# Kernel optimization log

Measured on AMD Instinct MI355X. Metric: run time of the kernel, lower is better.

## Reference

```python
import jax, jax.numpy as jnp
import numpy as np

N = 50000      # node_num
C = 64         # num_classes
G = 3          # number of metapath graphs (len(g))
E = 1200000    # edges per metapath graph
L = 2          # layers (PLPConv propagation steps)
D = 256        # input feature dim (feat_dims[0])
H = 256        # hidden_dim


def setup_inputs() -> dict:
    key = jax.random.key(0)
    ks = jax.random.split(key, 13)
    features0 = jax.random.normal(ks[0], (N, D), jnp.float32)
    labels = jax.random.randint(ks[1], (N,), 0, C)
    labels_one_hot = jax.nn.one_hot(labels, C, dtype=jnp.float32)
    # label_init: soft labels, rows on the simplex
    label_init = jax.nn.softmax(jax.random.normal(ks[2], (N, C), jnp.float32), axis=-1)
    train_mask = (jax.random.uniform(ks[3], (N, 1)) < 0.5).astype(jnp.float32)
    src = jax.random.randint(ks[4], (G, E), 0, N, dtype=jnp.int32)
    dst = jax.random.randint(ks[5], (G, E), 0, N, dtype=jnp.int32)
    # per-layer, per-graph learned edge logits (xavier-ish small init)
    e_edges = 0.1 * jax.random.normal(ks[6], (L, G, E), jnp.float32)
    attention = 0.5 * jax.random.normal(ks[7], (N, G), jnp.float32)
    alpha = 0.5 * jax.random.normal(ks[8], (N, 1), jnp.float32)
    W1 = jax.random.normal(ks[9], (D, H), jnp.float32) / np.sqrt(D)
    b1 = jnp.zeros((H,), jnp.float32)
    W2 = jax.random.normal(ks[10], (H, C), jnp.float32) / np.sqrt(H)
    b2 = jnp.zeros((C,), jnp.float32)
    return {"features0": features0, "label_init": label_init,
            "labels_one_hot": labels_one_hot, "train_mask": train_mask,
            "src": src, "dst": dst, "e_edges": e_edges,
            "attention": attention, "alpha": alpha,
            "W1": W1, "b1": b1, "W2": W2, "b2": b2}


def _edge_softmax(e, dst, n):
    # softmax of per-edge scalar over incoming edges of each dst node
    m = jax.ops.segment_max(e, dst, num_segments=n)
    a = jnp.exp(e - m[dst])
    s = jax.ops.segment_sum(a, dst, num_segments=n)
    return a / s[dst]


def reference(features0, label_init, labels_one_hot, train_mask,
              src, dst, e_edges, attention, alpha, W1, b1, W2, b2):
    n = label_init.shape[0]
    masked_label = 1.0 - train_mask            # (~masked).float(), [N,1]
    masked_oh = labels_one_hot * train_mask    # labels_one_hot * masked, [N,C]

    # Label propagation over each metapath graph (PLPConv stack, activation=None)
    h_prime = []
    for i in range(G):
        h = label_init
        for l in range(L):
            a = _edge_softmax(e_edges[l, i], dst[i], n)         # [E]
            msg = h[src[i]] * a[:, None]                        # gather-mul [E,C]
            h = jax.ops.segment_sum(msg, dst[i], num_segments=n)  # scatter-sum [N,C]
            h = h * masked_label + masked_oh                    # clamp train labels
        h_prime.append(h)
    x = jnp.stack(h_prime, axis=-1)                             # [N,C,G]

    att_mp = jax.nn.softmax(attention, axis=1)                  # [N,G]
    logits_lp = jnp.einsum('ncg,ng->nc', x, att_mp)             # [N,C]

    # MLP2 (2 layers, dropout=0): relu(x W1 + b1) W2 + b2
    hm = jax.nn.relu(features0 @ W1 + b1)
    logits_ns = hm @ W2 + b2                                    # [N,C]

    logits = jax.nn.sigmoid(alpha) * logits_lp + jax.nn.sigmoid(-alpha) * logits_ns
    return (logits, logits_lp, logits_ns)
```

## Files before the change

kernel.cpp:

```cpp
#include <hip/hip_runtime.h>
#include <hip/hip_bf16.h>

#define NN 50000
#define CC 64
#define GG 3
#define EE 1200000
#define LL 2
#define DD 256
#define HH 256
#define NB 196
#define NBLK 293
#define NBK (GG * NB)
#define BKCAP 8192
#define CH 16384
#define CBLK 74


__device__ __forceinline__ ushort f2bf(float f) {
    unsigned b = __float_as_uint(f);
    return (ushort)((b + 0x7fffu + ((b >> 16) & 1u)) >> 16);
}
__device__ __forceinline__ float bf2f(unsigned u) {
    return __uint_as_float(u << 16);
}

typedef __attribute__((ext_vector_type(8))) short s8v;
typedef __attribute__((ext_vector_type(4))) float f4v;

template<int NWM, int NWN, bool A_FP32, bool OUT_RELU_BF16>
__global__ __launch_bounds__(256) void mfma_gemm_kernel(
    const void* __restrict__ Av, const ushort* __restrict__ Bt,
    const float* __restrict__ bias, void* __restrict__ Cv, int M, int Nc)
{
    static_assert(NWM * NWN == 4, "4 waves per block");
    const int tid = threadIdx.x;
    const int w = tid >> 6;
    const int l = tid & 63;
    const int wm = w / NWN;
    const int wn = w % NWN;
    const int r0 = blockIdx.x * (NWM * 64) + wm * 64;
    const int c0 = blockIdx.y * (NWN * 64) + wn * 64;
    const int lrow = l & 15;
    const int lk = (l >> 4) << 3;

    f4v acc[4][4] = {};

    for (int k0 = 0; k0 < 256; k0 += 32) {
        s8v a[4], b[4];
        #pragma unroll
        for (int i = 0; i < 4; i++) {
            int row = r0 + lrow + 16 * i;
            row = (row < M) ? row : (M - 1);
            if constexpr (A_FP32) {
                const float* Af = (const float*)Av;
                const float4* p = (const float4*)(Af + (size_t)row * 256 + k0 + lk);
                float4 f0 = p[0], f1 = p[1];
                union { ushort u[8]; s8v v; } t;
                t.u[0] = f2bf(f0.x); t.u[1] = f2bf(f0.y);
                t.u[2] = f2bf(f0.z); t.u[3] = f2bf(f0.w);
                t.u[4] = f2bf(f1.x); t.u[5] = f2bf(f1.y);
                t.u[6] = f2bf(f1.z); t.u[7] = f2bf(f1.w);
                a[i] = t.v;
            } else {
                const ushort* Ab = (const ushort*)Av;
                a[i] = *(const s8v*)(Ab + (size_t)row * 256 + k0 + lk);
            }
        }
        #pragma unroll
        for (int j = 0; j < 4; j++) {
            int col = c0 + lrow + 16 * j;
            b[j] = *(const s8v*)(Bt + (size_t)col * 256 + k0 + lk);
        }
        #pragma unroll
        for (int i = 0; i < 4; i++)
            #pragma unroll
            for (int j = 0; j < 4; j++)
                acc[i][j] = __builtin_amdgcn_mfma_f32_16x16x32_bf16(
                    a[i], b[j], acc[i][j], 0, 0, 0);
    }

    #pragma unroll
    for (int i = 0; i < 4; i++) {
        #pragma unroll
        for (int r = 0; r < 4; r++) {
            int row = r0 + 16 * i + (l >> 4) * 4 + r;
            if (row >= M) continue;
            #pragma unroll
            for (int j = 0; j < 4; j++) {
                int col = c0 + 16 * j + lrow;
                float v = acc[i][j][r] + bias[col];
                if constexpr (OUT_RELU_BF16) {
                    v = fmaxf(v, 0.f);
                    ((ushort*)Cv)[(size_t)row * Nc + col] = f2bf(v);
                } else {
                    ((float*)Cv)[(size_t)row * Nc + col] = v;
                }
            }
        }
    }
}

__global__ void wcvt_kernel(const float* __restrict__ W1,
                            const float* __restrict__ W2,
                            ushort* __restrict__ Wt1, ushort* __restrict__ Wt2)
{
    int idx = blockIdx.x * 256 + threadIdx.x;
    if (idx < 256 * 256) {
        int n = idx >> 8, k = idx & 255;
        Wt1[idx] = f2bf(W1[k * 256 + n]);
    } else {
        int i = idx - 256 * 256;
        if (i < 64 * 256) {
            int n = i >> 8, k = i & 255;
            Wt2[i] = f2bf(W2[k * 64 + n]);
        }
    }
}

__global__ __launch_bounds__(256) void prep_kernel(
    const float* __restrict__ label_init, const float* __restrict__ labels_oh,
    const float* __restrict__ train_mask, ushort* __restrict__ lab_bf,
    short* __restrict__ mid)
{
    int b = blockIdx.x;
    if (b < 3125) {
        int i = b * 256 + threadIdx.x;
        int v = i >> 4;
        int c4 = (i & 15) * 4;
        float4 f = ((const float4*)label_init)[i];
        ushort4 u;
        u.x = f2bf(f.x); u.y = f2bf(f.y); u.z = f2bf(f.z); u.w = f2bf(f.w);
        int pl = c4 >> 5;
        *(ushort4*)(lab_bf + (size_t)pl * NN * 32 + (size_t)v * 32 + (c4 & 31)) = u;
    } else {
        int t = threadIdx.x;
        int v = (b - 3125) * 16 + (t >> 4);
        int sl = t & 15;
        if (v < NN) {
            float4 f = ((const float4*)(labels_oh + (size_t)v * 64))[sl];
            float p = (float)(sl * 4);
            float s = f.x * p + f.y * (p + 1.f) + f.z * (p + 2.f) + f.w * (p + 3.f);
            s += __shfl_xor(s, 1); s += __shfl_xor(s, 2);
            s += __shfl_xor(s, 4); s += __shfl_xor(s, 8);
            if (sl == 0) {
                float tm = train_mask[v];
                mid[v] = (tm > 0.5f) ? (short)(s + 0.5f) : (short)-1;
            }
        }
    }
}

__global__ __launch_bounds__(256) void bhist_kernel(
    const int* __restrict__ dst, int* __restrict__ bcnt)
{
    int blk = blockIdx.x;
    int g = blk / NBLK;
    int bi = blk - g * NBLK;
    int base = bi * 4096;
    __shared__ int cnt[NB];
    int t = threadIdx.x;
    if (t < NB) cnt[t] = 0;
    __syncthreads();
    #pragma unroll
    for (int k = 0; k < 16; k++) {
        int e = base + k * 256 + t;
        if (e < EE) atomicAdd(&cnt[dst[g * EE + e] >> 8], 1);
    }
    __syncthreads();
    if (t < NB && cnt[t] > 0) atomicAdd(&bcnt[g * NB + t], cnt[t]);
}

__global__ void scan_bucket(const int* __restrict__ bcnt, int* __restrict__ bs)
{
    __shared__ int sd[256];
    __shared__ int s_run;
    int t = threadIdx.x;
    if (t == 0) s_run = 0;
    __syncthreads();
    for (int base = 0; base < NBK; base += 256) {
        int i = base + t;
        int v = (i < NBK) ? bcnt[i] : 0;
        sd[t] = v;
        __syncthreads();
        for (int o = 1; o < 256; o <<= 1) {
            int x = (t >= o) ? sd[t - o] : 0;
            __syncthreads();
            sd[t] += x;
            __syncthreads();
        }
        int run = s_run;
        __syncthreads();
        if (i < NBK) bs[i] = run + sd[t] - v;
        if (t == 255) s_run = run + sd[255];
        __syncthreads();
    }
    if (t == 0) bs[NBK] = GG * EE;
}

__global__ __launch_bounds__(1024) void binA_kernel(
    const int* __restrict__ dst, const int* __restrict__ src,
    const float* __restrict__ e_edges, const int* __restrict__ bucket_start,
    int* __restrict__ fill, uint2* __restrict__ staging)
{
    int blk = blockIdx.x;
    int g = blk / CBLK;
    int bi = blk - g * CBLK;
    int base = bi * CH;
    __shared__ uint2 rec[CH];
    __shared__ int cnt[NB];
    __shared__ int lstart[NB];
    __shared__ int cur[NB];
    __shared__ int gbase[NB];
    __shared__ int sd[256];
    int t = threadIdx.x;
    if (t < NB) cnt[t] = 0;
    __syncthreads();

    int myd[16];
    #pragma unroll
    for (int k = 0; k < 16; k++) {
        int e = base + k * 1024 + t;
        int d = (e < EE) ? dst[g * EE + e] : -1;
        myd[k] = d;
        if (d >= 0) atomicAdd(&cnt[d >> 8], 1);
    }
    __syncthreads();

    if (t < 256) sd[t] = (t < NB) ? cnt[t] : 0;
    __syncthreads();
    for (int o = 1; o < 256; o <<= 1) {
        int x = (t < 256 && t >= o) ? sd[t - o] : 0;
        __syncthreads();
        if (t < 256) sd[t] += x;
        __syncthreads();
    }
    if (t < NB) {
        int c = cnt[t];
        int ls = sd[t] - c;
        lstart[t] = ls;
        cur[t] = ls;
        int fo = (c > 0) ? atomicAdd(&fill[g * NB + t], c) : 0;
        gbase[t] = bucket_start[g * NB + t] + fo;
    }
    __syncthreads();

    #pragma unroll
    for (int k = 0; k < 16; k++) {
        int d = myd[k];
        if (d >= 0) {
            int e = base + k * 1024 + t;
            int pos = atomicAdd(&cur[d >> 8], 1);
            int idxg = g * EE + e;
            uint2 r;
            r.x = ((unsigned)f2bf(e_edges[idxg]) << 16) |
                  (unsigned)f2bf(e_edges[(size_t)(GG + g) * EE + e]);
            r.y = ((unsigned)src[idxg] << 16) | (unsigned)(d & 255);
            rec[pos] = r;
        }
    }
    __syncthreads();

    int w = t >> 6, lane = t & 63;
    for (int b = w; b < NB; b += 16) {
        int c = cnt[b];
        int ls = lstart[b];
        uint2* dp = staging + gbase[b];
        for (int i = lane; i < c; i += 64) dp[i] = rec[ls + i];
    }
}

__global__ __launch_bounds__(1024) void bucket_kernel(
    const uint2* __restrict__ staging, const int* __restrict__ bucket_start,
    int* __restrict__ row_start, unsigned* __restrict__ packed0,
    unsigned* __restrict__ packed1)
{
    int blk = blockIdx.x;
    int g = blk / NB;
    int bucket = blk - g * NB;
    int bn = bucket << 8;
    int bnodes = min(256, NN - bn);
    int sbase = bucket_start[blk];
    int n = bucket_start[blk + 1] - sbase;
    int segStart = sbase - g * EE;
    const uint2* st = staging + sbase;

    __shared__ int hist[256];
    __shared__ int sd[256];
    __shared__ int cur[256];
    __shared__ float sm[512];
    __shared__ ushort ab0[BKCAP];
    __shared__ ushort ab1[BKCAP];
    __shared__ ushort sb[BKCAP];
    int t = threadIdx.x;
    if (t < 256) hist[t] = 0;
    if (t < 512) sm[t] = 0.f;
    __syncthreads();

    for (int i = t; i < n; i += 1024) {
        uint2 r = st[i];
        int dl = r.y & 0xff;
        atomicAdd(&hist[dl], 1);
        atomicAdd(&sm[dl], __expf(bf2f(r.x >> 16)));
        atomicAdd(&sm[256 + dl], __expf(bf2f(r.x & 0xffffu)));
    }
    __syncthreads();

    if (t < 256) sd[t] = hist[t];
    __syncthreads();
    for (int o = 1; o < 256; o <<= 1) {
        int x = (t < 256 && t >= o) ? sd[t - o] : 0;
        __syncthreads();
        if (t < 256) sd[t] += x;
        __syncthreads();
    }
    if (t < 256) {
        cur[t] = sd[t] - hist[t];
        if (t < bnodes)
            row_start[(size_t)g * (NN + 1) + bn + t] = segStart + sd[t] - hist[t];
        if (hist[t] > 0) {
            sm[t] = 1.f / sm[t];
            sm[256 + t] = 1.f / sm[256 + t];
        }
    }
    if (bucket == NB - 1 && t == 0) row_start[(size_t)g * (NN + 1) + NN] = EE;
    __syncthreads();

    for (int i = t; i < n; i += 1024) {
        uint2 r = st[i];
        int dl = r.y & 0xff;
        int pos = atomicAdd(&cur[dl], 1);
        ab0[pos] = f2bf(__expf(bf2f(r.x >> 16)) * sm[dl]);
        ab1[pos] = f2bf(__expf(bf2f(r.x & 0xffffu)) * sm[256 + dl]);
        sb[pos] = (ushort)(r.y >> 16);
    }
    __syncthreads();

    for (int i = t; i < n; i += 1024) {
        unsigned s = sb[i];
        packed0[(size_t)sbase + i] = ((unsigned)ab0[i] << 16) | s;
        packed1[(size_t)sbase + i] = ((unsigned)ab1[i] << 16) | s;
    }
}

__device__ __forceinline__ void tile_pass(unsigned packed, int cnt,
        const ushort* __restrict__ plane, unsigned loff, int sub, float acc[4])
{
    for (int q0 = 0; q0 < cnt; q0 += 32) {
        uint2 gv[4]; float w[4];
        #pragma unroll
        for (int u = 0; u < 4; u++) {
            unsigned pkq = __shfl(packed, q0 + 8 * u + sub);
            w[u] = __uint_as_float(pkq & 0xffff0000u);
            gv[u] = *(const uint2*)((const char*)plane +
                                    (((pkq & 0xffffu) << 6) | loff));
        }
        #pragma unroll
        for (int u = 0; u < 4; u++) {
            acc[0] = fmaf(__uint_as_float(gv[u].x << 16),          w[u], acc[0]);
            acc[1] = fmaf(__uint_as_float(gv[u].x & 0xffff0000u),  w[u], acc[1]);
            acc[2] = fmaf(__uint_as_float(gv[u].y << 16),          w[u], acc[2]);
            acc[3] = fmaf(__uint_as_float(gv[u].y & 0xffff0000u),  w[u], acc[3]);
        }
    }
}

__global__ __launch_bounds__(256) void prop0_kernel(
    const ushort* __restrict__ lab_bf, const short* __restrict__ mid,
    const int* __restrict__ row_start, const unsigned* __restrict__ packed0,
    ushort* __restrict__ h_buf)
{
    int wid = (blockIdx.x * blockDim.x + threadIdx.x) >> 6;
    int lane = threadIdx.x & 63;
    if (wid >= GG * NN) return;
    int g = wid / NN;
    int v = wid - g * NN;
    const int* rs = row_start + (size_t)g * (NN + 1);
    int s = rs[v], tE = rs[v + 1];
    const unsigned* pk = packed0 + (size_t)g * EE;
    const ushort* pl0 = lab_bf;
    const ushort* pl1 = lab_bf + (size_t)NN * 32;

    unsigned loff = (lane & 7) << 3;
    int sub = lane >> 3;
    float a0[4] = {}, a1[4] = {};
    for (int base = s; base < tE; base += 64) {
        int j = base + lane;
        unsigned packed = (j < tE) ? pk[j] : 0u;
        int cnt = min(64, tE - base);
        tile_pass(packed, cnt, pl0, loff, sub, a0);
        tile_pass(packed, cnt, pl1, loff, sub, a1);
    }
    #pragma unroll
    for (int c = 0; c < 4; c++) {
        a0[c] += __shfl_xor(a0[c], 8);
        a0[c] += __shfl_xor(a0[c], 16);
        a0[c] += __shfl_xor(a0[c], 32);
        a1[c] += __shfl_xor(a1[c], 8);
        a1[c] += __shfl_xor(a1[c], 16);
        a1[c] += __shfl_xor(a1[c], 32);
    }
    int m = mid[v];
    float ml = (m < 0) ? 1.f : 0.f;
    ushort* hg = h_buf + (size_t)g * NN * 64;
    int cb = (lane & 7) * 4;
    if (lane < 8) {
        ushort4 o;
        o.x = f2bf(a0[0] * ml + ((cb + 0 == m) ? 1.f : 0.f));
        o.y = f2bf(a0[1] * ml + ((cb + 1 == m) ? 1.f : 0.f));
        o.z = f2bf(a0[2] * ml + ((cb + 2 == m) ? 1.f : 0.f));
        o.w = f2bf(a0[3] * ml + ((cb + 3 == m) ? 1.f : 0.f));
        *(ushort4*)(hg + (size_t)v * 32 + cb) = o;
    } else if (lane < 16) {
        int cc = cb + 32;
        ushort4 o;
        o.x = f2bf(a1[0] * ml + ((cc + 0 == m) ? 1.f : 0.f));
        o.y = f2bf(a1[1] * ml + ((cc + 1 == m) ? 1.f : 0.f));
        o.z = f2bf(a1[2] * ml + ((cc + 2 == m) ? 1.f : 0.f));
        o.w = f2bf(a1[3] * ml + ((cc + 3 == m) ? 1.f : 0.f));
        *(ushort4*)(hg + (size_t)NN * 32 + (size_t)v * 32 + cb) = o;
    }
}

__global__ __launch_bounds__(256) void final_kernel(
    const ushort* __restrict__ h_buf, const short* __restrict__ mid,
    const float* __restrict__ attention, const float* __restrict__ alpha,
    const int* __restrict__ row_start, const unsigned* __restrict__ packed1,
    const float* __restrict__ out_ns, float* __restrict__ out_logits,
    float* __restrict__ out_lp)
{
    int wid = (blockIdx.x * blockDim.x + threadIdx.x) >> 6;
    int lane = threadIdx.x & 63;
    if (wid >= NN) return;
    int v = wid;
    float t0 = attention[v * 3], t1 = attention[v * 3 + 1], t2 = attention[v * 3 + 2];
    float mxa = fmaxf(t0, fmaxf(t1, t2));
    float e0 = __expf(t0 - mxa), e1 = __expf(t1 - mxa), e2 = __expf(t2 - mxa);
    float ainv = 1.f / (e0 + e1 + e2);
    float attw[3] = {e0 * ainv, e1 * ainv, e2 * ainv};

    unsigned loff = (lane & 7) << 3;
    int sub = lane >> 3;
    float w0[4] = {}, w1[4] = {};
    #pragma unroll
    for (int g = 0; g < GG; g++) {
        const int* rs = row_start + (size_t)g * (NN + 1);
        int s = rs[v], tE = rs[v + 1];
        const unsigned* pk = packed1 + (size_t)g * EE;
        const ushort* hp0 = h_buf + (size_t)g * NN * 64;
        const ushort* hp1 = hp0 + (size_t)NN * 32;
        float b0[4] = {}, b1[4] = {};
        for (int base = s; base < tE; base += 64) {
            int j = base + lane;
            unsigned packed = (j < tE) ? pk[j] : 0u;
            int cnt = min(64, tE - base);
            tile_pass(packed, cnt, hp0, loff, sub, b0);
            tile_pass(packed, cnt, hp1, loff, sub, b1);
        }
        float aw = attw[g];
        #pragma unroll
        for (int c = 0; c < 4; c++) {
            w0[c] = fmaf(aw, b0[c], w0[c]);
            w1[c] = fmaf(aw, b1[c], w1[c]);
        }
    }
    #pragma unroll
    for (int c = 0; c < 4; c++) {
        w0[c] += __shfl_xor(w0[c], 8);
        w0[c] += __shfl_xor(w0[c], 16);
        w0[c] += __shfl_xor(w0[c], 32);
        w1[c] += __shfl_xor(w1[c], 8);
        w1[c] += __shfl_xor(w1[c], 16);
        w1[c] += __shfl_xor(w1[c], 32);
    }
    int m = mid[v];
    float ml = (m < 0) ? 1.f : 0.f;
    if (lane < 16) {
        int pl = lane >> 3;
        int cb = (lane & 7) * 4 + pl * 32;
        float4 lpv;
        if (pl == 0) {
            lpv.x = w0[0] * ml + ((cb + 0 == m) ? 1.f : 0.f);
            lpv.y = w0[1] * ml + ((cb + 1 == m) ? 1.f : 0.f);
            lpv.z = w0[2] * ml + ((cb + 2 == m) ? 1.f : 0.f);
            lpv.w = w0[3] * ml + ((cb + 3 == m) ? 1.f : 0.f);
        } else {
            lpv.x = w1[0] * ml + ((cb + 0 == m) ? 1.f : 0.f);
            lpv.y = w1[1] * ml + ((cb + 1 == m) ? 1.f : 0.f);
            lpv.z = w1[2] * ml + ((cb + 2 == m) ? 1.f : 0.f);
            lpv.w = w1[3] * ml + ((cb + 3 == m) ? 1.f : 0.f);
        }
        size_t o = (size_t)v * 64 + cb;
        *(float4*)(out_lp + o) = lpv;
        float al = alpha[v];
        float sg = 1.f / (1.f + __expf(-al));
        float4 ns = *(const float4*)(out_ns + o);
        float4 lg;
        lg.x = sg * lpv.x + (1.f - sg) * ns.x;
        lg.y = sg * lpv.y + (1.f - sg) * ns.y;
        lg.z = sg * lpv.z + (1.f - sg) * ns.z;
        lg.w = sg * lpv.w + (1.f - sg) * ns.w;
        *(float4*)(out_logits + o) = lg;
    }
}

extern "C" void kernel_launch(void* const* d_in, const int* in_sizes, int n_in,
                              void* d_out, int out_size, void* d_ws, size_t ws_size,
                              hipStream_t stream)
{
    const float* features0  = (const float*)d_in[0];
    const float* label_init = (const float*)d_in[1];
    const float* labels_oh  = (const float*)d_in[2];
    const float* train_mask = (const float*)d_in[3];
    const int*   src        = (const int*)d_in[4];
    const int*   dst        = (const int*)d_in[5];
    const float* e_edges    = (const float*)d_in[6];
    const float* attention  = (const float*)d_in[7];
    const float* alpha      = (const float*)d_in[8];
    const float* W1         = (const float*)d_in[9];
    const float* b1         = (const float*)d_in[10];
    const float* W2         = (const float*)d_in[11];
    const float* b2         = (const float*)d_in[12];

    float* out        = (float*)d_out;
    float* out_logits = out;
    float* out_lp     = out + (size_t)NN * CC;
    float* out_ns     = out + 2 * (size_t)NN * CC;

    char* base = (char*)d_ws;
    size_t off = 0;
    auto alloc = [&](size_t bytes) -> void* {
        void* p = base + off;
        off = (off + bytes + 255) & ~(size_t)255;
        return p;
    };
    int*      bcnt         = (int*)alloc((size_t)NBK * sizeof(int));
    int*      fill         = (int*)alloc((size_t)NBK * sizeof(int));
    size_t    zero_bytes   = off;
    int*      bucket_start = (int*)alloc((size_t)(NBK + 1) * sizeof(int));
    int*      row_start    = (int*)alloc((size_t)GG * (NN + 1) * sizeof(int));
    uint2*    staging      = (uint2*)alloc((size_t)GG * EE * sizeof(uint2));
    unsigned* packed0      = (unsigned*)alloc((size_t)GG * EE * sizeof(unsigned));
    unsigned* packed1      = (unsigned*)alloc((size_t)GG * EE * sizeof(unsigned));
    ushort*   h_buf        = (ushort*)alloc((size_t)GG * NN * CC * sizeof(ushort));
    ushort*   lab_bf       = (ushort*)alloc((size_t)NN * CC * sizeof(ushort));
    short*    mid          = (short*)alloc((size_t)NN * sizeof(short));

    ushort* Wt1   = (ushort*)packed0;
    ushort* Wt2   = Wt1 + 256 * 256;
    ushort* hm_bf = (ushort*)staging;

    wcvt_kernel<<<(256 * 256 + 64 * 256) / 256, 256, 0, stream>>>(W1, W2, Wt1, Wt2);
    mfma_gemm_kernel<2, 2, true, true><<<dim3((NN + 127) / 128, 2), 256, 0, stream>>>(
        features0, Wt1, b1, hm_bf, NN, HH);
    mfma_gemm_kernel<4, 1, false, false><<<dim3((NN + 255) / 256, 1), 256, 0, stream>>>(
        hm_bf, Wt2, b2, out_ns, NN, CC);

    prep_kernel<<<6250, 256, 0, stream>>>(label_init, labels_oh, train_mask,
                                          lab_bf, mid);

    hipMemsetAsync(bcnt, 0, zero_bytes, stream);
    bhist_kernel<<<GG * NBLK, 256, 0, stream>>>(dst, bcnt);
    scan_bucket<<<1, 256, 0, stream>>>(bcnt, bucket_start);
    binA_kernel<<<GG * CBLK, 1024, 0, stream>>>(
        dst, src, e_edges, bucket_start, fill, staging);
    bucket_kernel<<<GG * NB, 1024, 0, stream>>>(
        staging, bucket_start, row_start, packed0, packed1);

    prop0_kernel<<<((size_t)GG * NN * 64 + 255) / 256, 256, 0, stream>>>(
        lab_bf, mid, row_start, packed0, h_buf);

    final_kernel<<<((size_t)NN * 64 + 255) / 256, 256, 0, stream>>>(
        h_buf, mid, attention, alpha, row_start, packed1,
        out_ns, out_logits, out_lp);
}
```

Measured before the change: 512.3 us.

## Drop histogram pass with fixed-capacity buckets; split propagation per graph and half-plane

Removes the separate dst-histogram kernel. Edges are binned into fixed-capacity staging slots per bucket (BKCAP), and the prefix scan runs after binning on the fill counts. The propagation kernels now assign one wave per (graph, node, 32-channel half-plane), with block indices interleaved so both halves of a node run close together. The final kernel writes per-graph attention-weighted partials that a new combine kernel sums. This trades an extra pass over the edges and a single serial gather loop for more parallel work, more launches, and an extra round-trip of partial results through memory. It also relies on no bucket exceeding BKCAP edges, which the random inputs make likely.

```diff
diff --git a/kernel.cpp b/kernel.cpp
--- a/kernel.cpp
+++ b/kernel.cpp
@@ -9,7 +9,6 @@
 #define DD 256
 #define HH 256
 #define NB 196
-#define NBLK 293
 #define NBK (GG * NB)
 #define BKCAP 8192
 #define CH 16384
@@ -150,27 +149,7 @@
     }
 }
 
-__global__ __launch_bounds__(256) void bhist_kernel(
-    const int* __restrict__ dst, int* __restrict__ bcnt)
-{
-    int blk = blockIdx.x;
-    int g = blk / NBLK;
-    int bi = blk - g * NBLK;
-    int base = bi * 4096;
-    __shared__ int cnt[NB];
-    int t = threadIdx.x;
-    if (t < NB) cnt[t] = 0;
-    __syncthreads();
-    #pragma unroll
-    for (int k = 0; k < 16; k++) {
-        int e = base + k * 256 + t;
-        if (e < EE) atomicAdd(&cnt[dst[g * EE + e] >> 8], 1);
-    }
-    __syncthreads();
-    if (t < NB && cnt[t] > 0) atomicAdd(&bcnt[g * NB + t], cnt[t]);
-}
-
-__global__ void scan_bucket(const int* __restrict__ bcnt, int* __restrict__ bs)
+__global__ void scan_bucket(const int* __restrict__ fill, int* __restrict__ bs)
 {
     __shared__ int sd[256];
     __shared__ int s_run;
@@ -179,7 +158,7 @@
     __syncthreads();
     for (int base = 0; base < NBK; base += 256) {
         int i = base + t;
-        int v = (i < NBK) ? bcnt[i] : 0;
+        int v = (i < NBK) ? fill[i] : 0;
         sd[t] = v;
         __syncthreads();
         for (int o = 1; o < 256; o <<= 1) {
@@ -199,8 +178,8 @@
 
 __global__ __launch_bounds__(1024) void binA_kernel(
     const int* __restrict__ dst, const int* __restrict__ src,
-    const float* __restrict__ e_edges, const int* __restrict__ bucket_start,
-    int* __restrict__ fill, uint2* __restrict__ staging)
+    const float* __restrict__ e_edges, int* __restrict__ fill,
+    uint2* __restrict__ staging)
 {
     int blk = blockIdx.x;
     int g = blk / CBLK;
@@ -240,7 +219,7 @@
         lstart[t] = ls;
         cur[t] = ls;
         int fo = (c > 0) ? atomicAdd(&fill[g * NB + t], c) : 0;
-        gbase[t] = bucket_start[g * NB + t] + fo;
+        gbase[t] = (g * NB + t) * BKCAP + fo;
     }
     __syncthreads();
 
@@ -264,25 +243,25 @@
     for (int b = w; b < NB; b += 16) {
         int c = cnt[b];
         int ls = lstart[b];
-        uint2* dp = staging + gbase[b];
+        uint2* dp = staging + (size_t)gbase[b];
         for (int i = lane; i < c; i += 64) dp[i] = rec[ls + i];
     }
 }
 
 __global__ __launch_bounds__(1024) void bucket_kernel(
-    const uint2* __restrict__ staging, const int* __restrict__ bucket_start,
-    int* __restrict__ row_start, unsigned* __restrict__ packed0,
-    unsigned* __restrict__ packed1)
+    const uint2* __restrict__ staging, const int* __restrict__ fill,
+    const int* __restrict__ out_start, int* __restrict__ row_start,
+    unsigned* __restrict__ packed0, unsigned* __restrict__ packed1)
 {
     int blk = blockIdx.x;
     int g = blk / NB;
     int bucket = blk - g * NB;
     int bn = bucket << 8;
     int bnodes = min(256, NN - bn);
-    int sbase = bucket_start[blk];
-    int n = bucket_start[blk + 1] - sbase;
-    int segStart = sbase - g * EE;
-    const uint2* st = staging + sbase;
+    int n = fill[blk];
+    int obase = out_start[blk];
+    int segStart = obase - g * EE;
+    const uint2* st = staging + (size_t)blk * BKCAP;
 
     __shared__ int hist[256];
     __shared__ int sd[256];
@@ -337,8 +316,8 @@
 
     for (int i = t; i < n; i += 1024) {
         unsigned s = sb[i];
-        packed0[(size_t)sbase + i] = ((unsigned)ab0[i] << 16) | s;
-        packed1[(size_t)sbase + i] = ((unsigned)ab1[i] << 16) | s;
+        packed0[(size_t)obase + i] = ((unsigned)ab0[i] << 16) | s;
+        packed1[(size_t)obase + i] = ((unsigned)ab1[i] << 16) | s;
     }
 }
 
@@ -369,138 +348,130 @@
     const int* __restrict__ row_start, const unsigned* __restrict__ packed0,
     ushort* __restrict__ h_buf)
 {
-    int wid = (blockIdx.x * blockDim.x + threadIdx.x) >> 6;
-    int lane = threadIdx.x & 63;
-    if (wid >= GG * NN) return;
-    int g = wid / NN;
-    int v = wid - g * NN;
+    int blk = blockIdx.x;
+    int x = blk & 7, q = blk >> 3;
+    int pl = x & 1;
+    int bIdx = q * 4 + (x >> 1);
+    int w = threadIdx.x >> 6, lane = threadIdx.x & 63;
+    int gv = bIdx * 4 + w;
+    int g = gv / NN;
+    int v = gv - g * NN;
     const int* rs = row_start + (size_t)g * (NN + 1);
     int s = rs[v], tE = rs[v + 1];
     const unsigned* pk = packed0 + (size_t)g * EE;
-    const ushort* pl0 = lab_bf;
-    const ushort* pl1 = lab_bf + (size_t)NN * 32;
+    const ushort* plane = lab_bf + (size_t)pl * NN * 32;
 
     unsigned loff = (lane & 7) << 3;
     int sub = lane >> 3;
-    float a0[4] = {}, a1[4] = {};
+    float a[4] = {};
     for (int base = s; base < tE; base += 64) {
         int j = base + lane;
-        unsigned packed = (j < tE) ? pk[j] : 0u;
+        unsigned packed = (j < tE) ? __builtin_nontemporal_load(pk + j) : 0u;
         int cnt = min(64, tE - base);
-        tile_pass(packed, cnt, pl0, loff, sub, a0);
-        tile_pass(packed, cnt, pl1, loff, sub, a1);
+        tile_pass(packed, cnt, plane, loff, sub, a);
     }
     #pragma unroll
     for (int c = 0; c < 4; c++) {
-        a0[c] += __shfl_xor(a0[c], 8);
-        a0[c] += __shfl_xor(a0[c], 16);
-        a0[c] += __shfl_xor(a0[c], 32);
-        a1[c] += __shfl_xor(a1[c], 8);
-        a1[c] += __shfl_xor(a1[c], 16);
-        a1[c] += __shfl_xor(a1[c], 32);
+        a[c] += __shfl_xor(a[c], 8);
+        a[c] += __shfl_xor(a[c], 16);
+        a[c] += __shfl_xor(a[c], 32);
     }
     int m = mid[v];
     float ml = (m < 0) ? 1.f : 0.f;
-    ushort* hg = h_buf + (size_t)g * NN * 64;
-    int cb = (lane & 7) * 4;
     if (lane < 8) {
+        int cb = lane * 4;
+        int cg = pl * 32 + cb;
         ushort4 o;
-        o.x = f2bf(a0[0] * ml + ((cb + 0 == m) ? 1.f : 0.f));
-        o.y = f2bf(a0[1] * ml + ((cb + 1 == m) ? 1.f : 0.f));
-        o.z = f2bf(a0[2] * ml + ((cb + 2 == m) ? 1.f : 0.f));
-        o.w = f2bf(a0[3] * ml + ((cb + 3 == m) ? 1.f : 0.f));
-        *(ushort4*)(hg + (size_t)v * 32 + cb) = o;
-    } else if (lane < 16) {
-        int cc = cb + 32;
-        ushort4 o;
-        o.x = f2bf(a1[0] * ml + ((cc + 0 == m) ? 1.f : 0.f));
-        o.y = f2bf(a1[1] * ml + ((cc + 1 == m) ? 1.f : 0.f));
-        o.z = f2bf(a1[2] * ml + ((cc + 2 == m) ? 1.f : 0.f));
-        o.w = f2bf(a1[3] * ml + ((cc + 3 == m) ? 1.f : 0.f));
-        *(ushort4*)(hg + (size_t)NN * 32 + (size_t)v * 32 + cb) = o;
-    }
-}
-
-__global__ __launch_bounds__(256) void final_kernel(
-    const ushort* __restrict__ h_buf, const short* __restrict__ mid,
-    const float* __restrict__ attention, const float* __restrict__ alpha,
+        o.x = f2bf(a[0] * ml + ((cg + 0 == m) ? 1.f : 0.f));
+        o.y = f2bf(a[1] * ml + ((cg + 1 == m) ? 1.f : 0.f));
+        o.z = f2bf(a[2] * ml + ((cg + 2 == m) ? 1.f : 0.f));
+        o.w = f2bf(a[3] * ml + ((cg + 3 == m) ? 1.f : 0.f));
+        *(ushort4*)(h_buf + ((size_t)(g * 2 + pl)) * NN * 32 + (size_t)v * 32 + cb) = o;
+    }
+}
+
+__global__ __launch_bounds__(256) void finalp_kernel(
+    const ushort* __restrict__ h_buf, const float* __restrict__ attention,
     const int* __restrict__ row_start, const unsigned* __restrict__ packed1,
-    const float* __restrict__ out_ns, float* __restrict__ out_logits,
-    float* __restrict__ out_lp)
-{
-    int wid = (blockIdx.x * blockDim.x + threadIdx.x) >> 6;
-    int lane = threadIdx.x & 63;
-    if (wid >= NN) return;
-    int v = wid;
+    float* __restrict__ partial)
+{
+    int blk = blockIdx.x;
+    int x = blk & 7, q = blk >> 3;
+    int combo, vblk;
+    if (x < 2) {
+        if (q >= 6250) return;
+        combo = x; vblk = q;
+    } else if (x < 6) {
+        combo = x; vblk = q;
+    } else {
+        if (q >= 6250) return;
+        combo = x - 6; vblk = 6250 + q;
+    }
+    int g = combo >> 1, pl = combo & 1;
+    int w = threadIdx.x >> 6, lane = threadIdx.x & 63;
+    int v = vblk * 4 + w;
+    const int* rs = row_start + (size_t)g * (NN + 1);
+    int s = rs[v], tE = rs[v + 1];
+    const unsigned* pk = packed1 + (size_t)g * EE;
+    const ushort* plane = h_buf + ((size_t)(g * 2 + pl)) * NN * 32;
+
     float t0 = attention[v * 3], t1 = attention[v * 3 + 1], t2 = attention[v * 3 + 2];
     float mxa = fmaxf(t0, fmaxf(t1, t2));
     float e0 = __expf(t0 - mxa), e1 = __expf(t1 - mxa), e2 = __expf(t2 - mxa);
     float ainv = 1.f / (e0 + e1 + e2);
-    float attw[3] = {e0 * ainv, e1 * ainv, e2 * ainv};
+    float aw = ((g == 0) ? e0 : (g == 1) ? e1 : e2) * ainv;
 
     unsigned loff = (lane & 7) << 3;
     int sub = lane >> 3;
-    float w0[4] = {}, w1[4] = {};
-    #pragma unroll
-    for (int g = 0; g < GG; g++) {
-        const int* rs = row_start + (size_t)g * (NN + 1);
-        int s = rs[v], tE = rs[v + 1];
-        const unsigned* pk = packed1 + (size_t)g * EE;
-        const ushort* hp0 = h_buf + (size_t)g * NN * 64;
-        const ushort* hp1 = hp0 + (size_t)NN * 32;
-        float b0[4] = {}, b1[4] = {};
-        for (int base = s; base < tE; base += 64) {
-            int j = base + lane;
-            unsigned packed = (j < tE) ? pk[j] : 0u;
-            int cnt = min(64, tE - base);
-            tile_pass(packed, cnt, hp0, loff, sub, b0);
-            tile_pass(packed, cnt, hp1, loff, sub, b1);
-        }
-        float aw = attw[g];
-        #pragma unroll
-        for (int c = 0; c < 4; c++) {
-            w0[c] = fmaf(aw, b0[c], w0[c]);
-            w1[c] = fmaf(aw, b1[c], w1[c]);
-        }
+    float a[4] = {};
+    for (int base = s; base < tE; base += 64) {
+        int j = base + lane;
+        unsigned packed = (j < tE) ? __builtin_nontemporal_load(pk + j) : 0u;
+        int cnt = min(64, tE - base);
+        tile_pass(packed, cnt, plane, loff, sub, a);
     }
     #pragma unroll
     for (int c = 0; c < 4; c++) {
-        w0[c] += __shfl_xor(w0[c], 8);
-        w0[c] += __shfl_xor(w0[c], 16);
-        w0[c] += __shfl_xor(w0[c], 32);
-        w1[c] += __shfl_xor(w1[c], 8);
-        w1[c] += __shfl_xor(w1[c], 16);
-        w1[c] += __shfl_xor(w1[c], 32);
-    }
+        a[c] += __shfl_xor(a[c], 8);
+        a[c] += __shfl_xor(a[c], 16);
+        a[c] += __shfl_xor(a[c], 32);
+    }
+    if (lane < 8) {
+        float4 o;
+        o.x = a[0] * aw; o.y = a[1] * aw; o.z = a[2] * aw; o.w = a[3] * aw;
+        *(float4*)(partial + ((size_t)g * NN + v) * 64 + pl * 32 + lane * 4) = o;
+    }
+}
+
+__global__ __launch_bounds__(256) void combine_kernel(
+    const float* __restrict__ partial, const short* __restrict__ mid,
+    const float* __restrict__ alpha, const float* __restrict__ out_ns,
+    float* __restrict__ out_logits, float* __restrict__ out_lp)
+{
+    int i = blockIdx.x * 256 + threadIdx.x;
+    int v = i >> 4;
+    int c4 = (i & 15) * 4;
+    size_t o = (size_t)v * 64 + c4;
+    float4 p0 = *(const float4*)(partial + o);
+    float4 p1 = *(const float4*)(partial + (size_t)NN * 64 + o);
+    float4 p2 = *(const float4*)(partial + (size_t)2 * NN * 64 + o);
     int m = mid[v];
     float ml = (m < 0) ? 1.f : 0.f;
-    if (lane < 16) {
-        int pl = lane >> 3;
-        int cb = (lane & 7) * 4 + pl * 32;
-        float4 lpv;
-        if (pl == 0) {
-            lpv.x = w0[0] * ml + ((cb + 0 == m) ? 1.f : 0.f);
-            lpv.y = w0[1] * ml + ((cb + 1 == m) ? 1.f : 0.f);
-            lpv.z = w0[2] * ml + ((cb + 2 == m) ? 1.f : 0.f);
-            lpv.w = w0[3] * ml + ((cb + 3 == m) ? 1.f : 0.f);
-        } else {
-            lpv.x = w1[0] * ml + ((cb + 0 == m) ? 1.f : 0.f);
-            lpv.y = w1[1] * ml + ((cb + 1 == m) ? 1.f : 0.f);
-            lpv.z = w1[2] * ml + ((cb + 2 == m) ? 1.f : 0.f);
-            lpv.w = w1[3] * ml + ((cb + 3 == m) ? 1.f : 0.f);
-        }
-        size_t o = (size_t)v * 64 + cb;
-        *(float4*)(out_lp + o) = lpv;
-        float al = alpha[v];
-        float sg = 1.f / (1.f + __expf(-al));
-        float4 ns = *(const float4*)(out_ns + o);
-        float4 lg;
-        lg.x = sg * lpv.x + (1.f - sg) * ns.x;
-        lg.y = sg * lpv.y + (1.f - sg) * ns.y;
-        lg.z = sg * lpv.z + (1.f - sg) * ns.z;
-        lg.w = sg * lpv.w + (1.f - sg) * ns.w;
-        *(float4*)(out_logits + o) = lg;
-    }
+    float4 lp;
+    lp.x = (p0.x + p1.x + p2.x) * ml + ((c4 + 0 == m) ? 1.f : 0.f);
+    lp.y = (p0.y + p1.y + p2.y) * ml + ((c4 + 1 == m) ? 1.f : 0.f);
+    lp.z = (p0.z + p1.z + p2.z) * ml + ((c4 + 2 == m) ? 1.f : 0.f);
+    lp.w = (p0.w + p1.w + p2.w) * ml + ((c4 + 3 == m) ? 1.f : 0.f);
+    *(float4*)(out_lp + o) = lp;
+    float al = alpha[v];
+    float sg = 1.f / (1.f + __expf(-al));
+    float4 ns = *(const float4*)(out_ns + o);
+    float4 lg;
+    lg.x = sg * lp.x + (1.f - sg) * ns.x;
+    lg.y = sg * lp.y + (1.f - sg) * ns.y;
+    lg.z = sg * lp.z + (1.f - sg) * ns.z;
+    lg.w = sg * lp.w + (1.f - sg) * ns.w;
+    *(float4*)(out_logits + o) = lg;
 }
 
 extern "C" void kernel_launch(void* const* d_in, const int* in_sizes, int n_in,
@@ -533,21 +504,21 @@
         off = (off + bytes + 255) & ~(size_t)255;
         return p;
     };
-    int*      bcnt         = (int*)alloc((size_t)NBK * sizeof(int));
     int*      fill         = (int*)alloc((size_t)NBK * sizeof(int));
     size_t    zero_bytes   = off;
-    int*      bucket_start = (int*)alloc((size_t)(NBK + 1) * sizeof(int));
+    int*      out_start    = (int*)alloc((size_t)(NBK + 1) * sizeof(int));
     int*      row_start    = (int*)alloc((size_t)GG * (NN + 1) * sizeof(int));
-    uint2*    staging      = (uint2*)alloc((size_t)GG * EE * sizeof(uint2));
+    uint2*    staging      = (uint2*)alloc((size_t)NBK * BKCAP * sizeof(uint2));
     unsigned* packed0      = (unsigned*)alloc((size_t)GG * EE * sizeof(unsigned));
     unsigned* packed1      = (unsigned*)alloc((size_t)GG * EE * sizeof(unsigned));
     ushort*   h_buf        = (ushort*)alloc((size_t)GG * NN * CC * sizeof(ushort));
     ushort*   lab_bf       = (ushort*)alloc((size_t)NN * CC * sizeof(ushort));
     short*    mid          = (short*)alloc((size_t)NN * sizeof(short));
 
-    ushort* Wt1   = (ushort*)packed0;
-    ushort* Wt2   = Wt1 + 256 * 256;
-    ushort* hm_bf = (ushort*)staging;
+    ushort* Wt1     = (ushort*)packed0;
+    ushort* Wt2     = Wt1 + 256 * 256;
+    ushort* hm_bf   = (ushort*)staging;
+    float*  partial = (float*)staging;
 
     wcvt_kernel<<<(256 * 256 + 64 * 256) / 256, 256, 0, stream>>>(W1, W2, Wt1, Wt2);
     mfma_gemm_kernel<2, 2, true, true><<<dim3((NN + 127) / 128, 2), 256, 0, stream>>>(
@@ -558,18 +529,17 @@
     prep_kernel<<<6250, 256, 0, stream>>>(label_init, labels_oh, train_mask,
                                           lab_bf, mid);
 
-    hipMemsetAsync(bcnt, 0, zero_bytes, stream);
-    bhist_kernel<<<GG * NBLK, 256, 0, stream>>>(dst, bcnt);
-    scan_bucket<<<1, 256, 0, stream>>>(bcnt, bucket_start);
-    binA_kernel<<<GG * CBLK, 1024, 0, stream>>>(
-        dst, src, e_edges, bucket_start, fill, staging);
+    hipMemsetAsync(fill, 0, zero_bytes, stream);
+    binA_kernel<<<GG * CBLK, 1024, 0, stream>>>(dst, src, e_edges, fill, staging);
+    scan_bucket<<<1, 256, 0, stream>>>(fill, out_start);
     bucket_kernel<<<GG * NB, 1024, 0, stream>>>(
-        staging, bucket_start, row_start, packed0, packed1);
-
-    prop0_kernel<<<((size_t)GG * NN * 64 + 255) / 256, 256, 0, stream>>>(
+        staging, fill, out_start, row_start, packed0, packed1);
+
+    prop0_kernel<<<9375 * 8, 256, 0, stream>>>(
         lab_bf, mid, row_start, packed0, h_buf);
 
-    final_kernel<<<((size_t)NN * 64 + 255) / 256, 256, 0, stream>>>(
-        h_buf, mid, attention, alpha, row_start, packed1,
-        out_ns, out_logits, out_lp);
-}
+    finalp_kernel<<<12500 * 8, 256, 0, stream>>>(
+        h_buf, attention, row_start, packed1, partial);
+    combine_kernel<<<3125, 256, 0, stream>>>(
+        partial, mid, alpha, out_ns, out_logits, out_lp);
+}
```

After: 562.7 us. 9.8% more time.
